# Optimization experiments

Hardware: AMD Instinct MI355X
Metric: run time of the kernel (lower is better)

The kernel has to match this reference:

```python
import jax, jax.numpy as jnp
import numpy as np

MARGIN = 1.0
ALPHA = 0.5
EPS = 1e-12  # sqrt-smoothing epsilon (keeps grads finite on the zero diagonal)


def _pairwise_d2(x):
    # x: [B, D] -> squared euclidean distance matrix [B, B]
    sq = jnp.sum(x * x, axis=-1)
    return jnp.maximum(sq[:, None] + sq[None, :] - 2.0 * (x @ x.T), 0.0)


def setup_inputs() -> dict:
    key = jax.random.key(0)
    k1, k2 = jax.random.split(key)
    N, B, D = 32, 1024, 1024
    outputs = jax.random.normal(k1, (N, B, D), dtype=jnp.float32)
    encode_sentences = jax.random.normal(k2, (B, D), dtype=jnp.float32)
    return {"outputs": outputs, "encode_sentences": encode_sentences}


def reference(outputs, encode_sentences):
    # outputs: [N, B, D] (N secrets, batch B, embed D); encode_sentences: [B, D]
    N, B, D = outputs.shape

    # --- sentence (distance-consistency) loss ---
    # original: mean_i MSE( pdist(outputs[i]), pdist(encode_sentences) )
    d_sent = jnp.sqrt(_pairwise_d2(encode_sentences) + EPS)          # [B, B]
    d_out = jnp.sqrt(jax.vmap(_pairwise_d2)(outputs) + EPS)          # [N, B, B]
    # mean over N of per-i means == global mean (all terms same size B*B)
    sentence_loss = jnp.mean((d_out - d_sent[None]) ** 2)

    # --- secret (pairwise margin) loss ---
    # original: sum_{i<j} mean_b relu(margin - ||outputs[i,b] - outputs[j,b]||)
    x = jnp.swapaxes(outputs, 0, 1)                                   # [B, N, D]
    sq = jnp.sum(x * x, axis=-1)                                      # [B, N]
    gram = jnp.einsum('bnd,bmd->bnm', x, x)                           # [B, N, N]
    d2 = jnp.maximum(sq[:, :, None] + sq[:, None, :] - 2.0 * gram, 0.0)
    d = jnp.sqrt(d2 + EPS)                                            # [B, N, N]
    hinge = jax.nn.relu(MARGIN - d)                                   # [B, N, N]
    upper = jnp.triu(jnp.ones((N, N), dtype=bool), k=1)               # i < j mask
    secret_distance = jnp.sum(jnp.where(upper[None], hinge, 0.0)) / B
    n_pairs = N * (N - 1) / 2.0
    secret_loss = secret_distance / n_pairs

    loss = ALPHA * sentence_loss + (1.0 - ALPHA) * secret_loss
    return (loss, sentence_loss, secret_loss)
```

## Files before the change

### kernel.cpp

```cpp
#include <hip/hip_runtime.h>
#include <hip/hip_bf16.h>

#define N_SEC 32
#define BDIM 1024
#define DDIM 1024

typedef __attribute__((ext_vector_type(8))) short bf16x8;
typedef __attribute__((ext_vector_type(4))) float f32x4;
typedef __attribute__((ext_vector_type(4))) int i32x4;

#define WAITVM(n) asm volatile("s_waitcnt vmcnt(" #n ")" ::: "memory")

__device__ __forceinline__ void pipe_barrier() {
    __builtin_amdgcn_s_barrier();
    asm volatile("" ::: "memory");
    __builtin_amdgcn_sched_barrier(0);
}

__device__ __forceinline__ unsigned pk2(float a, float b) {
    union { __hip_bfloat162 h; unsigned u; } cv;
    cv.h = __float22bfloat162_rn(make_float2(a, b));
    return cv.u;
}

__device__ __forceinline__ i32x4 pack8(float4 a, float4 b) {
    i32x4 r;
    r[0] = pk2(a.x, a.y); r[1] = pk2(a.z, a.w);
    r[2] = pk2(b.x, b.y); r[3] = pk2(b.z, b.w);
    return r;
}

__device__ __forceinline__ f32x4 mfma16(bf16x8 a, bf16x8 b, f32x4 c) {
    return __builtin_amdgcn_mfma_f32_16x16x32_bf16(a, b, c, 0, 0, 0);
}

__device__ __forceinline__ float wave_sum(float v) {
    #pragma unroll
    for (int off = 32; off > 0; off >>= 1) v += __shfl_down(v, off, 64);
    return v;
}

__device__ __forceinline__ void gload16(const unsigned short* g, unsigned short* l) {
    __builtin_amdgcn_global_load_lds(
        (const __attribute__((address_space(1))) unsigned int*)g,
        (__attribute__((address_space(3))) unsigned int*)l, 16, 0, 0);
}


__global__ void prep_k(const float* __restrict__ outp, const float* __restrict__ enc,
                       unsigned short* __restrict__ Xb, unsigned short* __restrict__ Eb,
                       float* __restrict__ sq_out, float* __restrict__ sq_enc) {
    int wid = threadIdx.x >> 6, l = threadIdx.x & 63;
    int r = blockIdx.x * 4 + wid;
    bool isOut = r < N_SEC * BDIM;
    const float* src = isOut ? (outp + (size_t)r * DDIM)
                             : (enc + (size_t)(r - N_SEC * BDIM) * DDIM);
    unsigned short* dst = isOut ? (Xb + (size_t)r * DDIM)
                                : (Eb + (size_t)(r - N_SEC * BDIM) * DDIM);
    const float4* s4 = (const float4*)src;
    float s = 0.f;
    #pragma unroll
    for (int h = 0; h < 2; ++h) {
        int c = l + h * 64;
        float4 v0 = s4[2 * c], v1 = s4[2 * c + 1];
        i32x4 p = pack8(v0, v1);
        *(i32x4*)&dst[c * 8] = p;
        #pragma unroll
        for (int e = 0; e < 4; ++e) {
            unsigned u = (unsigned)p[e];
            float a = __uint_as_float(u << 16);
            float b = __uint_as_float(u & 0xFFFF0000u);
            s += a * a + b * b;
        }
    }
    s = wave_sum(s);
    if (l == 0) { if (isOut) sq_out[r] = s; else sq_enc[r - N_SEC * BDIM] = s; }
}

template<int MODE>
__global__ void gram6_k(const unsigned short* __restrict__ Xb, const float* __restrict__ sqv,
                        const float* __restrict__ dsent_r, float* __restrict__ dsent_w,
                        float* __restrict__ partials) {
    int n, tile;
    if (MODE == 1) {
        int g = blockIdx.x;
        int xcd = g & 7, local = g >> 3;
        n = xcd * 4 + local / 36;
        tile = local % 36;
    } else { n = 0; tile = blockIdx.x; }
    int idx = tile, ti = 0;
    while (idx >= 8 - ti) { idx -= 8 - ti; ti++; }
    int tj = ti + idx;
    const unsigned short* Xn = Xb + (size_t)n * BDIM * DDIM;
    const float* sqn = sqv + n * BDIM;
    int i0 = ti * 128, j0 = tj * 128;
    bool diag = (ti == tj);

    __shared__ __align__(16) unsigned short Ash[2][4096];
    __shared__ __align__(16) unsigned short Bsh[2][4096];
    __shared__ float red[4];

    int t = threadIdx.x, wid = t >> 6, l = t & 63;
    int wr = wid >> 1, wc = wid & 1;
    bool dead = diag && (wr > wc);
    int cg = l >> 4, lr = l & 15;

    f32x4 acc[4][4];
    #pragma unroll
    for (int a = 0; a < 4; a++)
        #pragma unroll
        for (int c = 0; c < 4; c++) acc[a][c] = f32x4{0.f, 0.f, 0.f, 0.f};

    int eoffA[4], eoffB[4];
    #pragma unroll
    for (int f = 0; f < 4; f++) {
        int ra = wr * 64 + f * 16 + lr;
        eoffA[f] = ra * 32 + ((cg ^ ((ra >> 1) & 3)) * 8);
        int rb = wc * 64 + f * 16 + lr;
        eoffB[f] = rb * 32 + ((cg ^ ((rb >> 1) & 3)) * 8);
    }

    int rs = wid * 16 + (l >> 2);
    int cgs = (l & 3) ^ ((rs >> 1) & 3);
    const unsigned short* gA0 = Xn + (size_t)(i0 + rs) * DDIM + cgs * 8;
    const unsigned short* gA1 = gA0 + (size_t)64 * DDIM;
    const unsigned short* gB0 = Xn + (size_t)(j0 + rs) * DDIM + cgs * 8;
    const unsigned short* gB1 = gB0 + (size_t)64 * DDIM;

    auto stage = [&](int buf, int kt) {
        int ko = kt * 32;
        gload16(gA0 + ko, &Ash[buf][wid * 512]);
        gload16(gA1 + ko, &Ash[buf][2048 + wid * 512]);
        gload16(gB0 + ko, &Bsh[buf][wid * 512]);
        gload16(gB1 + ko, &Bsh[buf][2048 + wid * 512]);
    };
    auto compute = [&](int buf) {
        if (dead) return;
        bf16x8 af[4], bfr[4];
        #pragma unroll
        for (int f = 0; f < 4; f++) {
            af[f]  = *(const bf16x8*)&Ash[buf][eoffA[f]];
            bfr[f] = *(const bf16x8*)&Bsh[buf][eoffB[f]];
        }
        #pragma unroll
        for (int fi = 0; fi < 4; fi++)
            #pragma unroll
            for (int fj = 0; fj < 4; fj++) {
                if (diag && wr == wc && fj < fi) continue;
                acc[fi][fj] = mfma16(af[fi], bfr[fj], acc[fi][fj]);
            }
    };

#define GSTEP(NB, CB) do {                       \
        pipe_barrier();                          \
        int nx = c + 1; if (nx > 31) nx = 31;    \
        stage(NB, nx);                           \
        WAITVM(4);                               \
        compute(CB);                             \
        ++c; } while (0)

    stage(0, 0);
    int c = 0;
    #pragma unroll 1
    for (int it = 0; it < 16; ++it) {
        GSTEP(1, 0);
        GSTEP(0, 1);
    }
#undef GSTEP
    asm volatile("s_waitcnt vmcnt(0)" ::: "memory");

    float lsum = 0.f;
    if (!dead) {
        #pragma unroll
        for (int fi = 0; fi < 4; fi++) {
            #pragma unroll
            for (int fj = 0; fj < 4; fj++) {
                if (diag && wr == wc && fj < fi) continue;
                int jg = j0 + wc * 64 + fj * 16 + lr;
                #pragma unroll
                for (int e = 0; e < 4; e++) {
                    int ig = i0 + wr * 64 + fi * 16 + cg * 4 + e;
                    float g = acc[fi][fj][e];
                    float d2 = sqn[ig] + sqn[jg] - 2.f * g;
                    float d = sqrtf(fmaxf(d2, 0.f) + 1e-12f);
                    if (MODE == 0) {
                        dsent_w[(size_t)ig * BDIM + jg] = d;
                    } else {
                        if (!diag || jg > ig) {
                            float diff = d - dsent_r[(size_t)ig * BDIM + jg];
                            lsum += diff * diff;
                        }
                    }
                }
            }
        }
    }
    if (MODE == 1) {
        lsum = wave_sum(lsum * 2.f);
        if (l == 0) red[wid] = lsum;
        __syncthreads();
        if (t == 0) partials[blockIdx.x] = red[0] + red[1] + red[2] + red[3];
    }
}

__global__ void secret4_k(const unsigned short* __restrict__ Xb,
                          const float* __restrict__ sq_out, float* __restrict__ partials) {
    __shared__ __align__(16) unsigned short S[2][32 * 4 * 128];
    __shared__ float red[4];
    int t = threadIdx.x, wid = t >> 6, l = t & 63;
    int b0 = blockIdx.x * 4;
    int cg = l >> 4, lr = l & 15;
    f32x4 a00 = {0.f,0.f,0.f,0.f}, a01 = {0.f,0.f,0.f,0.f}, a11 = {0.f,0.f,0.f,0.f};

    auto stage = [&](int buf, int kt) {
        #pragma unroll
        for (int m = 0; m < 8; ++m) {
            int n = m * 4 + wid;
            gload16(Xb + ((size_t)(n * BDIM + b0 + cg)) * DDIM + kt * 128 + ((lr ^ (n & 7)) * 8),
                    &S[buf][n * 512]);
        }
    };
    auto compute = [&](int buf) {
        #pragma unroll
        for (int k2 = 0; k2 < 4; ++k2) {
            int cs = k2 * 4 + cg;
            int cl = (cs ^ (lr & 7)) * 8;
            bf16x8 u0 = *(const bf16x8*)&S[buf][lr * 512 + wid * 128 + cl];
            bf16x8 u1 = *(const bf16x8*)&S[buf][(16 + lr) * 512 + wid * 128 + cl];
            a00 = mfma16(u0, u0, a00);
            a01 = mfma16(u0, u1, a01);
            a11 = mfma16(u1, u1, a11);
        }
    };

    stage(0, 0);
    __syncthreads();
    for (int kt = 0; kt < 6; kt += 2) {
        stage(1, kt + 1);
        compute(0);
        __syncthreads();
        stage(0, kt + 2);
        compute(1);
        __syncthreads();
    }
    stage(1, 7);
    compute(0);
    __syncthreads();
    compute(1);

    float lsum = 0.f;
    int b = b0 + wid;
    auto proc = [&](const f32x4& acc, int rb, int cb) {
        #pragma unroll
        for (int e = 0; e < 4; e++) {
            int i = rb * 16 + cg * 4 + e;
            int j = cb * 16 + lr;
            if (j > i) {
                float d2 = sq_out[(size_t)i * BDIM + b] + sq_out[(size_t)j * BDIM + b] - 2.f * acc[e];
                float d = sqrtf(fmaxf(d2, 0.f) + 1e-12f);
                lsum += fmaxf(1.f - d, 0.f);
            }
        }
    };
    proc(a00, 0, 0); proc(a01, 0, 1); proc(a11, 1, 1);
    lsum = wave_sum(lsum);
    if (l == 0) red[wid] = lsum;
    __syncthreads();
    if (t == 0) partials[blockIdx.x] = red[0] + red[1] + red[2] + red[3];
}

__global__ void fin2_k(const float* __restrict__ ps, const float* __restrict__ psec,
                       float* __restrict__ out) {
    __shared__ float red[16];
    int t = threadIdx.x;
    float s = 0.f;
    for (int i = t; i < 36 * N_SEC; i += 256) s += ps[i];
    float s2 = psec[t];
    s = wave_sum(s);
    s2 = wave_sum(s2);
    if ((t & 63) == 0) { red[t >> 6] = s; red[8 + (t >> 6)] = s2; }
    __syncthreads();
    if (t == 0) {
        float a = red[0] + red[1] + red[2] + red[3];
        float b = red[8] + red[9] + red[10] + red[11];
        float sl = a * (1.0f / 33554432.0f);
        float sec = b * (1.0f / (1024.0f * 496.0f));
        out[0] = 0.5f * sl + 0.5f * sec;
        out[1] = sl;
        out[2] = sec;
    }
}


__global__ void norms_k(const float* __restrict__ outp, const float* __restrict__ enc,
                        float* __restrict__ sq_out, float* __restrict__ sq_enc) {
    int wid = threadIdx.x >> 6, l = threadIdx.x & 63;
    int r = blockIdx.x * 4 + wid;
    const float* src = (r < N_SEC * BDIM) ? (outp + (size_t)r * DDIM)
                                          : (enc + (size_t)(r - N_SEC * BDIM) * DDIM);
    float s = 0.f;
    #pragma unroll
    for (int q = 0; q < 4; q++) {
        float4 v = reinterpret_cast<const float4*>(src)[l + q * 64];
        unsigned u0 = pk2(v.x, v.y), u1 = pk2(v.z, v.w);
        float a = __uint_as_float(u0 << 16), b = __uint_as_float(u0 & 0xFFFF0000u);
        float c = __uint_as_float(u1 << 16), d = __uint_as_float(u1 & 0xFFFF0000u);
        s += a * a + b * b + c * c + d * d;
    }
    s = wave_sum(s);
    if (l == 0) { if (r < N_SEC * BDIM) sq_out[r] = s; else sq_enc[r - N_SEC * BDIM] = s; }
}

template<int MODE>
__global__ void gram_k(const float* __restrict__ X, const float* __restrict__ sqv,
                       const float* __restrict__ dsent_r, float* __restrict__ dsent_w,
                       float* __restrict__ accum) {
    int idx = blockIdx.x, ti = 0;
    while (idx >= 8 - ti) { idx -= 8 - ti; ti++; }
    int tj = ti + idx;
    int n = (MODE == 1) ? blockIdx.y : 0;
    const float* Xn = X + (size_t)n * BDIM * DDIM;
    const float* sqn = sqv + n * BDIM;
    int i0 = ti * 128, j0 = tj * 128;
    bool diag = (ti == tj);
    __shared__ __align__(16) unsigned short Ash[128 * 32];
    __shared__ __align__(16) unsigned short Bsh[128 * 32];
    int t = threadIdx.x, wid = t >> 6, l = t & 63;
    int wr = wid >> 1, wc = wid & 1;
    bool dead = diag && (wr > wc);
    int cg = l >> 4, lr = l & 15;
    f32x4 acc[4][4];
    #pragma unroll
    for (int a = 0; a < 4; a++)
        #pragma unroll
        for (int c = 0; c < 4; c++) acc[a][c] = f32x4{0.f, 0.f, 0.f, 0.f};
    int r0 = t >> 2, c0 = t & 3;
    int swz0 = (c0 ^ (r0 & 3)) * 8;
    int off0 = r0 * 32 + swz0;
    int off1 = (r0 + 64) * 32 + swz0;
    for (int kt = 0; kt < DDIM / 32; ++kt) {
        int k0 = kt * 32;
        const float4* pa0 = (const float4*)(Xn + (size_t)(i0 + r0) * DDIM + k0 + c0 * 8);
        const float4* pa1 = (const float4*)(Xn + (size_t)(i0 + r0 + 64) * DDIM + k0 + c0 * 8);
        const float4* pb0 = (const float4*)(Xn + (size_t)(j0 + r0) * DDIM + k0 + c0 * 8);
        const float4* pb1 = (const float4*)(Xn + (size_t)(j0 + r0 + 64) * DDIM + k0 + c0 * 8);
        float4 a00 = pa0[0], a01 = pa0[1];
        float4 a10 = pa1[0], a11 = pa1[1];
        float4 b00 = pb0[0], b01 = pb0[1];
        float4 b10 = pb1[0], b11 = pb1[1];
        __syncthreads();
        *(i32x4*)&Ash[off0] = pack8(a00, a01);
        *(i32x4*)&Ash[off1] = pack8(a10, a11);
        *(i32x4*)&Bsh[off0] = pack8(b00, b01);
        *(i32x4*)&Bsh[off1] = pack8(b10, b11);
        __syncthreads();
        if (!dead) {
            bf16x8 af[4], bfr[4];
            #pragma unroll
            for (int f = 0; f < 4; f++) {
                int ra = wr * 64 + f * 16 + lr;
                af[f] = *(const bf16x8*)&Ash[ra * 32 + ((cg ^ (ra & 3)) * 8)];
                int rb = wc * 64 + f * 16 + lr;
                bfr[f] = *(const bf16x8*)&Bsh[rb * 32 + ((cg ^ (rb & 3)) * 8)];
            }
            #pragma unroll
            for (int fi = 0; fi < 4; fi++)
                #pragma unroll
                for (int fj = 0; fj < 4; fj++) {
                    if (diag && wr == wc && fj < fi) continue;
                    acc[fi][fj] = mfma16(af[fi], bfr[fj], acc[fi][fj]);
                }
        }
    }
    if (!dead) {
        float lsum = 0.f;
        #pragma unroll
        for (int fi = 0; fi < 4; fi++) {
            #pragma unroll
            for (int fj = 0; fj < 4; fj++) {
                if (diag && wr == wc && fj < fi) continue;
                int jg = j0 + wc * 64 + fj * 16 + lr;
                #pragma unroll
                for (int e = 0; e < 4; e++) {
                    int ig = i0 + wr * 64 + fi * 16 + cg * 4 + e;
                    float g = acc[fi][fj][e];
                    float d2 = sqn[ig] + sqn[jg] - 2.f * g;
                    float d = sqrtf(fmaxf(d2, 0.f) + 1e-12f);
                    if (MODE == 0) {
                        dsent_w[(size_t)ig * BDIM + jg] = d;
                    } else {
                        if (!diag || jg > ig) {
                            float diff = d - dsent_r[(size_t)ig * BDIM + jg];
                            lsum += diff * diff;
                        }
                    }
                }
            }
        }
        if (MODE == 1) {
            lsum = wave_sum(lsum * 2.f);
            if (l == 0) atomicAdd(accum, lsum);
        }
    }
}

__global__ void secret_k(const float* __restrict__ X, const float* __restrict__ sq_out,
                         float* __restrict__ accum) {
    int wid = threadIdx.x >> 6, l = threadIdx.x & 63;
    int b = blockIdx.x * 4 + wid;
    int cg = l >> 4, lr = l & 15;
    f32x4 a00 = {0.f,0.f,0.f,0.f}, a01 = {0.f,0.f,0.f,0.f}, a11 = {0.f,0.f,0.f,0.f};
    for (int kt = 0; kt < 32; ++kt) {
        int k0 = kt * 32 + cg * 8;
        const float4* p0 = (const float4*)(X + ((size_t)lr * BDIM + b) * DDIM + k0);
        const float4* p1 = (const float4*)(X + ((size_t)(16 + lr) * BDIM + b) * DDIM + k0);
        union { i32x4 i; bf16x8 s; } u0, u1;
        u0.i = pack8(p0[0], p0[1]);
        u1.i = pack8(p1[0], p1[1]);
        a00 = mfma16(u0.s, u0.s, a00);
        a01 = mfma16(u0.s, u1.s, a01);
        a11 = mfma16(u1.s, u1.s, a11);
    }
    float lsum = 0.f;
    auto proc = [&](const f32x4& acc, int rb, int cb) {
        #pragma unroll
        for (int e = 0; e < 4; e++) {
            int i = rb * 16 + cg * 4 + e;
            int j = cb * 16 + lr;
            if (j > i) {
                float d2 = sq_out[(size_t)i * BDIM + b] + sq_out[(size_t)j * BDIM + b] - 2.f * acc[e];
                float d = sqrtf(fmaxf(d2, 0.f) + 1e-12f);
                lsum += fmaxf(1.f - d, 0.f);
            }
        }
    };
    proc(a00, 0, 0); proc(a01, 0, 1); proc(a11, 1, 1);
    lsum = wave_sum(lsum);
    if (l == 0) atomicAdd(accum, lsum);
}

__global__ void init_k(float* sums) { sums[threadIdx.x] = 0.f; }

__global__ void fin_k(const float* __restrict__ sums, float* __restrict__ out) {
    float sl = sums[0] * (1.0f / 33554432.0f);
    float sec = sums[1] * (1.0f / (1024.0f * 496.0f));
    out[0] = 0.5f * sl + 0.5f * sec;
    out[1] = sl;
    out[2] = sec;
}

extern "C" void kernel_launch(void* const* d_in, const int* in_sizes, int n_in,
                              void* d_out, int out_size, void* d_ws, size_t ws_size,
                              hipStream_t stream) {
    const float* outputs = (const float*)d_in[0];
    const float* enc     = (const float*)d_in[1];
    float* out = (float*)d_out;

    float* ps     = (float*)d_ws;
    float* psec   = ps + 1536;
    float* sq_out = ps + 2048;
    float* sq_enc = sq_out + N_SEC * BDIM;
    float* dsent  = sq_enc + BDIM;
    unsigned short* Xbf = (unsigned short*)(dsent + (size_t)BDIM * BDIM);
    unsigned short* Ebf = Xbf + (size_t)N_SEC * BDIM * DDIM;

    const size_t NEED = 4 * (2048 + (size_t)N_SEC * BDIM + BDIM + (size_t)BDIM * BDIM)
                      + 2 * ((size_t)N_SEC * BDIM * DDIM + (size_t)BDIM * DDIM);

    if (ws_size >= NEED) {
        hipLaunchKernelGGL(prep_k, dim3((N_SEC * BDIM + BDIM) / 4), dim3(256), 0, stream,
                           outputs, enc, Xbf, Ebf, sq_out, sq_enc);
        hipLaunchKernelGGL((gram6_k<0>), dim3(36), dim3(256), 0, stream,
                           Ebf, sq_enc, (const float*)nullptr, dsent, (float*)nullptr);
        hipLaunchKernelGGL((gram6_k<1>), dim3(36 * N_SEC), dim3(256), 0, stream,
                           Xbf, sq_out, (const float*)dsent, (float*)nullptr, ps);
        hipLaunchKernelGGL(secret4_k, dim3(BDIM / 4), dim3(256), 0, stream,
                           Xbf, sq_out, psec);
        hipLaunchKernelGGL(fin2_k, dim3(1), dim3(256), 0, stream, ps, psec, out);
    } else {
        float* sums = (float*)d_ws;
        float* fsq_out = sums + 64;
        float* fsq_enc = fsq_out + N_SEC * BDIM;
        float* fdsent  = fsq_enc + BDIM;
        hipLaunchKernelGGL(init_k, dim3(1), dim3(2), 0, stream, sums);
        hipLaunchKernelGGL(norms_k, dim3((N_SEC * BDIM + BDIM) / 4), dim3(256), 0, stream,
                           outputs, enc, fsq_out, fsq_enc);
        hipLaunchKernelGGL((gram_k<0>), dim3(36), dim3(256), 0, stream,
                           enc, fsq_enc, (const float*)nullptr, fdsent, (float*)nullptr);
        hipLaunchKernelGGL((gram_k<1>), dim3(36, N_SEC), dim3(256), 0, stream,
                           outputs, fsq_out, (const float*)fdsent, (float*)nullptr, &sums[0]);
        hipLaunchKernelGGL(secret_k, dim3(BDIM / 4), dim3(256), 0, stream,
                           outputs, fsq_out, &sums[1]);
        hipLaunchKernelGGL(fin_k, dim3(1), dim3(1), 0, stream, sums, out);
    }
}
```

Before: 154.1 us.

## Split-K the sentence Gram kernel and triple-buffer the LDS pipeline

The sentence-embedding Gram matrix, which previously ran on only 36 blocks, is now split four ways along K into 144 blocks. Their partial dot products are accumulated with atomicAdd into a pre-zeroed buffer, and a separate elementwise kernel then converts that buffer into distances. The shared Gram kernel also moves from double to triple LDS buffering, placing the barrier after the vmcnt wait and dropping the sched_barrier. In exchange it adds two extra kernel launches, float atomics whose summation order is not deterministic, and more LDS per block.

```diff
diff --git a/kernel.cpp b/kernel.cpp
--- a/kernel.cpp
+++ b/kernel.cpp
@@ -11,10 +11,9 @@
 
 #define WAITVM(n) asm volatile("s_waitcnt vmcnt(" #n ")" ::: "memory")
 
-__device__ __forceinline__ void pipe_barrier() {
+__device__ __forceinline__ void bar() {
     __builtin_amdgcn_s_barrier();
     asm volatile("" ::: "memory");
-    __builtin_amdgcn_sched_barrier(0);
 }
 
 __device__ __forceinline__ unsigned pk2(float a, float b) {
@@ -77,17 +76,48 @@
     if (l == 0) { if (isOut) sq_out[r] = s; else sq_enc[r - N_SEC * BDIM] = s; }
 }
 
-template<int MODE>
-__global__ void gram6_k(const unsigned short* __restrict__ Xb, const float* __restrict__ sqv,
+__global__ void zero_k(float* __restrict__ p) {
+    int i = blockIdx.x * blockDim.x + threadIdx.x;
+    float4 z = {0.f, 0.f, 0.f, 0.f};
+    ((float4*)p)[i] = z;
+    ((float4*)p)[i + 131072] = z;
+}
+
+__global__ void cvt0_k(float* __restrict__ d, const float* __restrict__ sq) {
+    int t = blockIdx.x * blockDim.x + threadIdx.x;
+    #pragma unroll
+    for (int h = 0; h < 2; ++h) {
+        int idx = t + h * 131072;
+        int i = idx >> 8;
+        float si = sq[i];
+        float4 g = ((const float4*)d)[idx];
+        int j0 = (idx & 255) * 4;
+        float4 r;
+        r.x = sqrtf(fmaxf(si + sq[j0 + 0] - 2.f * g.x, 0.f) + 1e-12f);
+        r.y = sqrtf(fmaxf(si + sq[j0 + 1] - 2.f * g.y, 0.f) + 1e-12f);
+        r.z = sqrtf(fmaxf(si + sq[j0 + 2] - 2.f * g.z, 0.f) + 1e-12f);
+        r.w = sqrtf(fmaxf(si + sq[j0 + 3] - 2.f * g.w, 0.f) + 1e-12f);
+        ((float4*)d)[idx] = r;
+    }
+}
+
+template<int MODE, int NIT>
+__global__ void gram8_k(const unsigned short* __restrict__ Xb, const float* __restrict__ sqv,
                         const float* __restrict__ dsent_r, float* __restrict__ dsent_w,
-                        float* __restrict__ partials) {
-    int n, tile;
+                        float* __restrict__ partials, int kbeg_base) {
+    int n, tile, kbeg;
     if (MODE == 1) {
         int g = blockIdx.x;
         int xcd = g & 7, local = g >> 3;
         n = xcd * 4 + local / 36;
         tile = local % 36;
-    } else { n = 0; tile = blockIdx.x; }
+        kbeg = 0;
+    } else {
+        n = 0;
+        tile = blockIdx.x >> 2;
+        kbeg = (blockIdx.x & 3) * NIT;
+        (void)kbeg_base;
+    }
     int idx = tile, ti = 0;
     while (idx >= 8 - ti) { idx -= 8 - ti; ti++; }
     int tj = ti + idx;
@@ -96,8 +126,8 @@
     int i0 = ti * 128, j0 = tj * 128;
     bool diag = (ti == tj);
 
-    __shared__ __align__(16) unsigned short Ash[2][4096];
-    __shared__ __align__(16) unsigned short Bsh[2][4096];
+    __shared__ __align__(16) unsigned short Ash[3][4096];
+    __shared__ __align__(16) unsigned short Bsh[3][4096];
     __shared__ float red[4];
 
     int t = threadIdx.x, wid = t >> 6, l = t & 63;
@@ -151,21 +181,25 @@
             }
     };
 
-#define GSTEP(NB, CB) do {                       \
-        pipe_barrier();                          \
-        int nx = c + 1; if (nx > 31) nx = 31;    \
-        stage(NB, nx);                           \
+    int klast = kbeg + NIT - 1;
+#define GSTEP(SB, CB) do {                       \
+        int nx = c + 1; if (nx > klast) nx = klast; \
+        stage(SB, nx);                           \
         WAITVM(4);                               \
+        bar();                                   \
         compute(CB);                             \
         ++c; } while (0)
 
-    stage(0, 0);
-    int c = 0;
+    stage(0, kbeg);
+    int c = kbeg;
     #pragma unroll 1
-    for (int it = 0; it < 16; ++it) {
+    for (int it = 0; it < NIT / 3; ++it) {
         GSTEP(1, 0);
-        GSTEP(0, 1);
-    }
+        GSTEP(2, 1);
+        GSTEP(0, 2);
+    }
+    if (NIT % 3 >= 1) GSTEP(1, 0);
+    if (NIT % 3 >= 2) GSTEP(2, 1);
 #undef GSTEP
     asm volatile("s_waitcnt vmcnt(0)" ::: "memory");
 
@@ -181,11 +215,11 @@
                 for (int e = 0; e < 4; e++) {
                     int ig = i0 + wr * 64 + fi * 16 + cg * 4 + e;
                     float g = acc[fi][fj][e];
-                    float d2 = sqn[ig] + sqn[jg] - 2.f * g;
-                    float d = sqrtf(fmaxf(d2, 0.f) + 1e-12f);
-                    if (MODE == 0) {
-                        dsent_w[(size_t)ig * BDIM + jg] = d;
+                    if (MODE == 2) {
+                        atomicAdd(&dsent_w[(size_t)ig * BDIM + jg], g);
                     } else {
+                        float d2 = sqn[ig] + sqn[jg] - 2.f * g;
+                        float d = sqrtf(fmaxf(d2, 0.f) + 1e-12f);
                         if (!diag || jg > ig) {
                             float diff = d - dsent_r[(size_t)ig * BDIM + jg];
                             lsum += diff * diff;
@@ -470,10 +504,12 @@
     if (ws_size >= NEED) {
         hipLaunchKernelGGL(prep_k, dim3((N_SEC * BDIM + BDIM) / 4), dim3(256), 0, stream,
                            outputs, enc, Xbf, Ebf, sq_out, sq_enc);
-        hipLaunchKernelGGL((gram6_k<0>), dim3(36), dim3(256), 0, stream,
-                           Ebf, sq_enc, (const float*)nullptr, dsent, (float*)nullptr);
-        hipLaunchKernelGGL((gram6_k<1>), dim3(36 * N_SEC), dim3(256), 0, stream,
-                           Xbf, sq_out, (const float*)dsent, (float*)nullptr, ps);
+        hipLaunchKernelGGL(zero_k, dim3(512), dim3(256), 0, stream, dsent);
+        hipLaunchKernelGGL((gram8_k<2, 8>), dim3(36 * 4), dim3(256), 0, stream,
+                           Ebf, sq_enc, (const float*)nullptr, dsent, (float*)nullptr, 0);
+        hipLaunchKernelGGL(cvt0_k, dim3(512), dim3(256), 0, stream, dsent, sq_enc);
+        hipLaunchKernelGGL((gram8_k<1, 32>), dim3(36 * N_SEC), dim3(256), 0, stream,
+                           Xbf, sq_out, (const float*)dsent, (float*)nullptr, ps, 0);
         hipLaunchKernelGGL(secret4_k, dim3(BDIM / 4), dim3(256), 0, stream,
                            Xbf, sq_out, psec);
         hipLaunchKernelGGL(fin2_k, dim3(1), dim3(256), 0, stream, ps, psec, out);
```

Measured after the change: 146.9 us, median of 2. -4.7%, faster.
